# Kernel tuning notes

Hardware: AMD Instinct MI355X
Metric: run time of the kernel (lower is better)

The kernel has to match this reference:

```python
import jax, jax.numpy as jnp
import numpy as np

K_WIN = 7  # temporal window size (odd)
EPS = 1e-5


def setup_inputs() -> dict:
    key = jax.random.key(0)
    ks = jax.random.split(key, 10)
    B, C, T, H, W = 8, 512, 32, 7, 7
    N, E = 8, 64  # heads, inter channels = C // N
    s = 0.02
    return {
        "x": jax.random.normal(ks[0], (B, C, T, H, W), jnp.float32),
        "gamma": jnp.ones((C,), jnp.float32),
        "beta": jnp.zeros((C,), jnp.float32),
        "Wq": jax.random.normal(ks[1], (N, E, C), jnp.float32) * s,
        "bq": jax.random.normal(ks[2], (N, E), jnp.float32) * s,
        "Wk": jax.random.normal(ks[3], (N, E, C), jnp.float32) * s,
        "bk": jax.random.normal(ks[4], (N, E), jnp.float32) * s,
        "Wv": jax.random.normal(ks[5], (N, E, C), jnp.float32) * s,
        "bv": jax.random.normal(ks[6], (N, E), jnp.float32) * s,
        "Wo": jax.random.normal(ks[7], (N, C, E), jnp.float32) * s,
        "bo": jax.random.normal(ks[8], (N, C), jnp.float32) * s,
    }


def reference(x, gamma, beta, Wq, bq, Wk, bk, Wv, bv, Wo, bo):
    B, C, T, H, W = x.shape
    K = K_WIN
    P = H * W          # spatial positions per frame
    L = K * P          # positions per temporal window

    # BatchNorm3d (training-mode batch stats over B,T,H,W)
    mean = jnp.mean(x, axis=(0, 2, 3, 4), keepdims=True)
    var = jnp.var(x, axis=(0, 2, 3, 4), keepdims=True)
    g = gamma[None, :, None, None, None]
    b = beta[None, :, None, None, None]
    xb = g * (x - mean) * jax.lax.rsqrt(var + EPS) + b  # (B,C,T,H,W)

    # temporal zero-pad so that number of windows S == T
    pad = K // 2
    xp = jnp.pad(xb, ((0, 0), (0, 0), (pad, pad), (0, 0), (0, 0)))
    # gather sliding windows: (B,C,T,K,H,W)
    win_idx = jnp.arange(T)[:, None] + jnp.arange(K)[None, :]
    xw = xp[:, :, win_idx]

    xwf = xw.reshape(B, C, T, L)   # window tokens (key/value source)
    xcf = xb.reshape(B, C, T, P)   # center frame (query source)

    # per-head projections (dropout is identity in eval mode)
    q = jnp.einsum('nec,bctp->bntep', Wq, xcf) + bq[None, :, None, :, None]
    k = jnp.einsum('nec,bctl->bntel', Wk, xwf) + bk[None, :, None, :, None]
    v = jnp.einsum('nec,bctl->bntel', Wv, xwf) + bv[None, :, None, :, None]

    # attention: scores (B,N,T,P,L), softmax over window positions L (no scaling, as in original)
    alpha = jnp.einsum('bntep,bntel->bntpl', q, k)
    alpha = jax.nn.softmax(alpha, axis=-1)
    y = jnp.einsum('bntpl,bntel->bntep', alpha, v)

    # output projection per head, then mean over heads
    out = jnp.einsum('nce,bntep->bntcp', Wo, y) + bo[None, :, None, :, None]
    z = jnp.mean(out, axis=1)                 # (B,T,C,P)
    z = jnp.transpose(z, (0, 2, 1, 3)).reshape(B, C, T, H, W)
    return z + xb  # residual with BN output
```

## Files before the change

kernel.cpp:

```cpp
#include <hip/hip_runtime.h>
#include <hip/hip_bf16.h>


typedef float f32x4 __attribute__((ext_vector_type(4)));
typedef float f32x2 __attribute__((ext_vector_type(2)));
typedef short s16x8 __attribute__((ext_vector_type(8)));
typedef short s16x4 __attribute__((ext_vector_type(4)));
typedef __bf16 bf16x8 __attribute__((ext_vector_type(8)));

static __device__ __forceinline__ float bf2f(unsigned short u){
  union { unsigned int i; float f; } x; x.i = ((unsigned int)u) << 16; return x.f;
}
static __device__ __forceinline__ unsigned short f2bf(float f){
  union { __hip_bfloat16 h; unsigned short u; } x; x.h = __float2bfloat16(f); return x.u;
}
static __device__ __forceinline__ f32x4 mfma16(s16x8 a, s16x8 b, f32x4 c){
  return __builtin_amdgcn_mfma_f32_16x16x32_bf16(
      __builtin_bit_cast(bf16x8, a), __builtin_bit_cast(bf16x8, b), c, 0, 0, 0);
}
static __device__ __forceinline__ void gload16(const unsigned short* g, unsigned short* l){
  __builtin_amdgcn_global_load_lds(
      (const __attribute__((address_space(1))) unsigned int*)g,
      (__attribute__((address_space(3))) unsigned int*)l, 16, 0, 0);
}

__global__ __launch_bounds__(256) void xt_kernel(const float* __restrict__ x,
    unsigned short* __restrict__ Xt){
  __shared__ unsigned short Xc[512][53];
  const int bt = blockIdx.x, b = bt >> 5, t = bt & 31, tid = threadIdx.x;
  const float* xb = x + (size_t)b*802816 + t*49;
  for (int i = tid; i < 512*49; i += 256){
    int c = i / 49, p = i - c*49;
    Xc[c][p] = f2bf(xb[(size_t)c*1568 + p]);
  }
  __syncthreads();
  unsigned short* dst = Xt + (size_t)bt*49*512;
  for (int i = tid; i < 49*64; i += 256){
    int p = i >> 6, c0 = (i & 63) << 3;
    s16x8 v;
    #pragma unroll
    for (int j = 0; j < 8; ++j) v[j] = (short)Xc[c0+j][p];
    *(s16x8*)(dst + p*512 + c0) = v;
  }
}

__global__ __launch_bounds__(256) void stats1_kernel(const unsigned short* __restrict__ Xt,
    float* __restrict__ partials){
  __shared__ float R1[4][512];
  __shared__ float R2[4][512];
  const int blk = blockIdx.x, tid = threadIdx.x;
  const int rt = tid >> 6, c0 = (tid & 63)*8;
  const int r0 = blk*128;
  float s1[8] = {0,0,0,0,0,0,0,0}, s2[8] = {0,0,0,0,0,0,0,0};
  for (int r = rt; r < 128; r += 4){
    s16x8 v = *(const s16x8*)(Xt + (size_t)(r0 + r)*512 + c0);
    #pragma unroll
    for (int j = 0; j < 8; ++j){
      float f = bf2f((unsigned short)v[j]);
      s1[j] += f; s2[j] += f*f;
    }
  }
  #pragma unroll
  for (int j = 0; j < 8; ++j){ R1[rt][c0+j] = s1[j]; R2[rt][c0+j] = s2[j]; }
  __syncthreads();
  for (int c = tid; c < 512; c += 256){
    f32x2 o;
    o[0] = R1[0][c]+R1[1][c]+R1[2][c]+R1[3][c];
    o[1] = R2[0][c]+R2[1][c]+R2[2][c]+R2[3][c];
    *(f32x2*)(partials + ((size_t)blk*512 + c)*2) = o;
  }
}

__global__ __launch_bounds__(512) void stats2_kernel(const float* __restrict__ partials,
    const float* __restrict__ gamma, const float* __restrict__ beta,
    float* __restrict__ scale, float* __restrict__ shift){
  const int c = threadIdx.x;
  float s1 = 0.f, s2 = 0.f;
  for (int k = 0; k < 98; ++k){
    f32x2 v = *(const f32x2*)(partials + ((size_t)k*512 + c)*2);
    s1 += v[0]; s2 += v[1];
  }
  const float inv = 1.f/12544.f;
  float mean = s1*inv;
  float var  = s2*inv - mean*mean;
  float sc = gamma[c]*rsqrtf(var + 1e-5f);
  scale[c] = sc;
  shift[c] = beta[c] - mean*sc;
}

__global__ __launch_bounds__(512) void pack_kernel(const float* __restrict__ Wq,
    const float* __restrict__ Wk, const float* __restrict__ Wv,
    const float* __restrict__ Wo, const float* __restrict__ bo,
    const float* __restrict__ scale,
    unsigned short* __restrict__ Wall, unsigned short* __restrict__ Wo2,
    float* __restrict__ bo_sum){
  int i = blockIdx.x*512 + threadIdx.x;
  if (i < 786432){
    const float* W = (i < 262144) ? Wq : (i < 524288 ? Wk : Wv);
    Wall[i] = f2bf(W[i & 262143] * scale[i & 511]);
  } else if (i < 1048576){
    int j = i - 786432;
    int c = j >> 9, k = j & 511, nn = k >> 6, e = k & 63;
    Wo2[j] = f2bf(Wo[((size_t)nn*512 + c)*64 + e] * 0.125f);
  } else if (i < 1049088){
    int c = i - 1048576;
    float s = 0.f;
    #pragma unroll
    for (int nn = 0; nn < 8; ++nn) s += bo[nn*512 + c];
    bo_sum[c] = s * 0.125f;
  }
}

__global__ __launch_bounds__(64) void bias_kernel(const float* __restrict__ Wq,
    const float* __restrict__ Wk, const float* __restrict__ Wv,
    const float* __restrict__ bq, const float* __restrict__ bk,
    const float* __restrict__ bv, const float* __restrict__ shift,
    float* __restrict__ biasAll){
  const int row = blockIdx.x, lane = threadIdx.x;
  const float* W    = row < 512 ? Wq : (row < 1024 ? Wk : Wv);
  const float* bsrc = row < 512 ? bq : (row < 1024 ? bk : bv);
  const int r = row & 511;
  const float* Wr = W + (size_t)r*512;
  float s = 0.f;
  #pragma unroll
  for (int j = 0; j < 8; ++j) s += Wr[lane + 64*j]*shift[lane + 64*j];
  #pragma unroll
  for (int off = 32; off > 0; off >>= 1) s += __shfl_down(s, off);
  if (lane == 0) biasAll[row] = bsrc[r] + s;
}

__global__ __launch_bounds__(256) void qkv_gemm(const unsigned short* __restrict__ Wall,
    const unsigned short* __restrict__ Xt, const float* __restrict__ biasAll,
    unsigned short* __restrict__ Qg, unsigned short* __restrict__ Kg,
    unsigned short* __restrict__ Vg){
  __shared__ unsigned short As[2][4096];
  __shared__ unsigned short Bs[2][4096];
  const int bid = blockIdx.x;
  const int id = (bid & 7)*147 + (bid >> 3);
  const int bm = id % 12, bn = id / 12;
  const int m0 = bm*128, n0 = bn*128;
  const int tid = threadIdx.x;
  const int w = __builtin_amdgcn_readfirstlane(tid >> 6);
  const int lane = tid & 63, l15 = lane & 15, g = lane >> 4, g4 = (lane >> 4)*4;
  const int wm = w >> 1, wn = w & 1;
  const int cA = w*128 + lane;
  int offA[4], offB[4];
  #pragma unroll
  for (int mi = 0; mi < 4; ++mi){
    int row = wm*64 + mi*16 + l15;
    offA[mi] = row*32 + ((g ^ ((row>>1)&3))<<3);
  }
  #pragma unroll
  for (int ni = 0; ni < 4; ++ni){
    int col = wn*64 + ni*16 + l15;
    offB[ni] = col*32 + ((g ^ ((col>>1)&3))<<3);
  }
  f32x4 acc[4][4];
  #pragma unroll
  for (int mi = 0; mi < 4; ++mi)
    #pragma unroll
    for (int ni = 0; ni < 4; ++ni) acc[mi][ni] = 0.f;

  auto stage = [&](int bufi, int ks){
    #pragma unroll
    for (int it = 0; it < 2; ++it){
      int c = cA + it*64;
      int row = c >> 2, slot = c & 3;
      int ko = ks*32 + ((slot ^ ((row>>1)&3))<<3);
      gload16(Wall + (size_t)(m0 + row)*512 + ko, &As[bufi][(w*128 + it*64)*8]);
      gload16(Xt   + (size_t)(n0 + row)*512 + ko, &Bs[bufi][(w*128 + it*64)*8]);
    }
  };
  auto compute = [&](int bufi){
    s16x8 Af[4], Bf[4];
    #pragma unroll
    for (int mi = 0; mi < 4; ++mi) Af[mi] = *(const s16x8*)&As[bufi][offA[mi]];
    #pragma unroll
    for (int ni = 0; ni < 4; ++ni) Bf[ni] = *(const s16x8*)&Bs[bufi][offB[ni]];
    #pragma unroll
    for (int mi = 0; mi < 4; ++mi)
      #pragma unroll
      for (int ni = 0; ni < 4; ++ni)
        acc[mi][ni] = mfma16(Af[mi], Bf[ni], acc[mi][ni]);
  };

  stage(0, 0);
  __syncthreads();
  #pragma unroll 1
  for (int kk = 0; kk < 8; ++kk){
    stage(1, kk*2 + 1);
    compute(0);
    __syncthreads();
    if (kk < 7) stage(0, kk*2 + 2);
    compute(1);
    __syncthreads();
  }

  const int qb = bm*2 + wm;
  const int which = qb >> 3, n = qb & 7;
  f32x4 bb[4];
  #pragma unroll
  for (int mi = 0; mi < 4; ++mi)
    bb[mi] = *(const f32x4*)(biasAll + qb*64 + mi*16 + g4);
  #pragma unroll
  for (int ni = 0; ni < 4; ++ni){
    const int col = n0 + wn*64 + ni*16 + l15;
    const int btc = col / 49, p = col - btc*49;
    const size_t bnt = ((size_t)((btc >> 5)*8 + n)*32 + (btc & 31));
    #pragma unroll
    for (int mi = 0; mi < 4; ++mi){
      const int e0 = mi*16 + g4;
      f32x4 v = acc[mi][ni] + bb[mi];
      if (which == 0) v *= 1.4426950408889634f;
      if (which < 2){
        s16x4 u;
        #pragma unroll
        for (int r = 0; r < 4; ++r) u[r] = (short)f2bf(v[r]);
        *(s16x4*)((which == 0 ? Qg : Kg) + (bnt*49 + p)*64 + e0) = u;
      } else {
        #pragma unroll
        for (int r = 0; r < 4; ++r)
          Vg[bnt*3328 + (size_t)(e0 + r)*52 + p] = f2bf(v[r]);
      }
    }
  }
}

__global__ __launch_bounds__(512,2) void attn_kernel(const unsigned short* __restrict__ Qg,
    const unsigned short* __restrict__ Kg, const unsigned short* __restrict__ Vg,
    const float* __restrict__ bk, const float* __restrict__ bv,
    unsigned short* __restrict__ Yg){
  const int bid = blockIdx.x;
  const int bt = ((bid & 7) << 5) | (bid >> 3);
  const int b = bt >> 5, t = bt & 31, tid = threadIdx.x;
  const int n = __builtin_amdgcn_readfirstlane(tid >> 6);
  const int lane = tid & 63, g = lane >> 4, l15 = lane & 15, g4 = (lane >> 4)*4;
  const size_t bnt = ((size_t)(b*8 + n)*32 + t);
  const unsigned short* Qb = Qg + bnt*3136;
  s16x8 Qf[4][2];
  #pragma unroll
  for (int ni = 0; ni < 4; ++ni)
    #pragma unroll
    for (int ks = 0; ks < 2; ++ks)
      Qf[ni][ks] = *(const s16x8*)(Qb + (ni*16 + l15)*64 + ks*32 + g*8);
  const float* bkp = bk + n*64;
  f32x4 bkf[2][2];
  bkf[0][0] = *(const f32x4*)(bkp + g*8);      bkf[0][1] = *(const f32x4*)(bkp + g*8 + 4);
  bkf[1][0] = *(const f32x4*)(bkp + 32 + g*8); bkf[1][1] = *(const f32x4*)(bkp + 32 + g*8 + 4);
  float pad_l[4];
  #pragma unroll
  for (int ni = 0; ni < 4; ++ni){
    float s = 0.f;
    #pragma unroll
    for (int ks = 0; ks < 2; ++ks)
      #pragma unroll
      for (int h = 0; h < 2; ++h)
        #pragma unroll
        for (int j = 0; j < 4; ++j)
          s += bf2f((unsigned short)Qf[ni][ks][h*4+j]) * bkf[ks][h][j];
    s += __shfl_xor(s, 16); s += __shfl_xor(s, 32);
    pad_l[ni] = s;
  }
  float m_run[4], d_run[4];
  f32x4 Yacc[4][4];
  #pragma unroll
  for (int ni = 0; ni < 4; ++ni){
    m_run[ni] = -1e30f; d_run[ni] = 0.f;
    #pragma unroll
    for (int me = 0; me < 4; ++me) Yacc[me][ni] = 0.f;
  }
  int slo = 3 - t; if (slo < 0) slo = 0;
  int shi = 34 - t; if (shi > 6) shi = 6;
  for (int s = slo; s <= shi; ++s){
    const int tt = t + s - 3;
    const unsigned short* Kb = Kg + ((size_t)(b*8 + n)*32 + tt)*3136;
    const unsigned short* Vb = Vg + ((size_t)(b*8 + n)*32 + tt)*3328;
    f32x4 S[4][4];
    #pragma unroll
    for (int mi = 0; mi < 4; ++mi)
      #pragma unroll
      for (int ni = 0; ni < 4; ++ni) S[mi][ni] = 0.f;
    __builtin_amdgcn_s_setprio(1);
    #pragma unroll
    for (int ks = 0; ks < 2; ++ks)
      #pragma unroll
      for (int mi = 0; mi < 4; ++mi){
        s16x8 Kf = *(const s16x8*)(Kb + (mi*16 + l15)*64 + ks*32 + g*8);
        #pragma unroll
        for (int ni = 0; ni < 4; ++ni)
          S[mi][ni] = mfma16(Kf, Qf[ni][ks], S[mi][ni]);
      }
    __builtin_amdgcn_s_setprio(0);
    #pragma unroll
    for (int r = 0; r < 4; ++r){
      const bool bad = (g4 + r) >= 1;
      #pragma unroll
      for (int ni = 0; ni < 4; ++ni)
        S[3][ni][r] = bad ? -1e30f : S[3][ni][r];
    }
    #pragma unroll
    for (int ni = 0; ni < 4; ++ni){
      float mx = -1e30f;
      #pragma unroll
      for (int mi = 0; mi < 4; ++mi)
        #pragma unroll
        for (int r = 0; r < 4; ++r) mx = fmaxf(mx, S[mi][ni][r]);
      mx = fmaxf(mx, __shfl_xor(mx, 16));
      mx = fmaxf(mx, __shfl_xor(mx, 32));
      const float mn = fmaxf(m_run[ni], mx);
      const float rs = exp2f(m_run[ni] - mn);
      m_run[ni] = mn;
      float sum = 0.f;
      #pragma unroll
      for (int mi = 0; mi < 4; ++mi)
        #pragma unroll
        for (int r = 0; r < 4; ++r){
          float e = exp2f(S[mi][ni][r] - mn);
          S[mi][ni][r] = e; sum += e;
        }
      sum += __shfl_xor(sum, 16); sum += __shfl_xor(sum, 32);
      d_run[ni] = d_run[ni]*rs + sum;
      #pragma unroll
      for (int me = 0; me < 4; ++me) Yacc[me][ni] *= rs;
    }
    #pragma unroll
    for (int ks = 0; ks < 2; ++ks){
      s16x8 Pf[4];
      #pragma unroll
      for (int ni = 0; ni < 4; ++ni){
        f32x4 a = S[2*ks][ni], b2 = S[2*ks+1][ni];
        s16x8 pf;
        #pragma unroll
        for (int j = 0; j < 4; ++j){
          pf[j]   = (short)f2bf(a[j]);
          pf[4+j] = (short)f2bf(b2[j]);
        }
        Pf[ni] = pf;
      }
      __builtin_amdgcn_s_setprio(1);
      #pragma unroll
      for (int me = 0; me < 4; ++me){
        s16x4 vlo = *(const s16x4*)(Vb + (size_t)(me*16 + l15)*52 + ks*32 + g4);
        s16x4 vhi = *(const s16x4*)(Vb + (size_t)(me*16 + l15)*52 + ks*32 + 16 + g4);
        s16x8 Vf;
        #pragma unroll
        for (int j = 0; j < 4; ++j){ Vf[j] = vlo[j]; Vf[4+j] = vhi[j]; }
        #pragma unroll
        for (int ni = 0; ni < 4; ++ni)
          Yacc[me][ni] = mfma16(Vf, Pf[ni], Yacc[me][ni]);
      }
      __builtin_amdgcn_s_setprio(0);
    }
  }
  const int n_pad = slo + (6 - shi);
  f32x4 bvf[4];
  #pragma unroll
  for (int me = 0; me < 4; ++me)
    bvf[me] = *(const f32x4*)(bv + n*64 + me*16 + g4);
  unsigned short* Yb = Yg + bnt*3136;
  #pragma unroll
  for (int ni = 0; ni < 4; ++ni){
    float rs = 1.f, pw = 0.f, d = d_run[ni];
    if (n_pad > 0){
      const float mf = fmaxf(m_run[ni], pad_l[ni]);
      rs = exp2f(m_run[ni] - mf);
      pw = (float)(n_pad*49) * exp2f(pad_l[ni] - mf);
      d = d_run[ni]*rs + pw;
    }
    const float inv = 1.f/d;
    const int p = ni*16 + l15;
    if (p < 49){
      #pragma unroll
      for (int me = 0; me < 4; ++me){
        s16x4 u;
        #pragma unroll
        for (int r = 0; r < 4; ++r)
          u[r] = (short)f2bf((Yacc[me][ni][r]*rs + pw*bvf[me][r])*inv);
        *(s16x4*)(Yb + (size_t)p*64 + me*16 + g4) = u;
      }
    }
  }
}

__global__ __launch_bounds__(256) void out_gemm(const unsigned short* __restrict__ Wo2,
    const unsigned short* __restrict__ Yg, const unsigned short* __restrict__ Xt,
    const float* __restrict__ scale, const float* __restrict__ shift,
    const float* __restrict__ bo_sum, float* __restrict__ out){
  __shared__ unsigned short As[2][4096];
  __shared__ unsigned short Bs[2][4096];
  const int bid = blockIdx.x;
  const int id = (bid & 7)*49 + (bid >> 3);
  const int bm = id % 4, bn = id / 4;
  const int m0 = bm*128, n0 = bn*128;
  const int tid = threadIdx.x;
  const int w = __builtin_amdgcn_readfirstlane(tid >> 6);
  const int lane = tid & 63, l15 = lane & 15, g = lane >> 4, g4 = (lane >> 4)*4;
  const int wm = w >> 1, wn = w & 1;
  const int cA = w*128 + lane;
  int offA[4], offB[4];
  #pragma unroll
  for (int mi = 0; mi < 4; ++mi){
    int row = wm*64 + mi*16 + l15;
    offA[mi] = row*32 + ((g ^ ((row>>1)&3))<<3);
  }
  #pragma unroll
  for (int ni = 0; ni < 4; ++ni){
    int col = wn*64 + ni*16 + l15;
    offB[ni] = col*32 + ((g ^ ((col>>1)&3))<<3);
  }
  f32x4 acc[4][4];
  #pragma unroll
  for (int mi = 0; mi < 4; ++mi)
    #pragma unroll
    for (int ni = 0; ni < 4; ++ni) acc[mi][ni] = 0.f;

  auto stage = [&](int bufi, int ks){
    const int nh = ks >> 1, eo = (ks & 1)*32;
    #pragma unroll
    for (int it = 0; it < 2; ++it){
      int c = cA + it*64;
      int row = c >> 2, slot = c & 3;
      int sw = ((slot ^ ((row>>1)&3))<<3);
      gload16(Wo2 + (size_t)(m0 + row)*512 + ks*32 + sw, &As[bufi][(w*128 + it*64)*8]);
      const int col = n0 + row;
      const int btc = col / 49, p = col - btc*49;
      const size_t bb = ((size_t)((btc >> 5)*8 + nh)*32 + (btc & 31));
      gload16(Yg + bb*3136 + p*64 + eo + sw, &Bs[bufi][(w*128 + it*64)*8]);
    }
  };
  auto compute = [&](int bufi){
    s16x8 Af[4], Bf[4];
    #pragma unroll
    for (int mi = 0; mi < 4; ++mi) Af[mi] = *(const s16x8*)&As[bufi][offA[mi]];
    #pragma unroll
    for (int ni = 0; ni < 4; ++ni) Bf[ni] = *(const s16x8*)&Bs[bufi][offB[ni]];
    #pragma unroll
    for (int mi = 0; mi < 4; ++mi)
      #pragma unroll
      for (int ni = 0; ni < 4; ++ni)
        acc[mi][ni] = mfma16(Af[mi], Bf[ni], acc[mi][ni]);
  };

  stage(0, 0);
  __syncthreads();
  #pragma unroll 1
  for (int kk = 0; kk < 8; ++kk){
    stage(1, kk*2 + 1);
    compute(0);
    __syncthreads();
    if (kk < 7) stage(0, kk*2 + 2);
    compute(1);
    __syncthreads();
  }

  const int cb = m0 + wm*64;
  int colv[4]; size_t obase[4];
  #pragma unroll
  for (int ni = 0; ni < 4; ++ni){
    const int col = n0 + wn*64 + ni*16 + l15;
    const int btc = col / 49, p = col - btc*49;
    const int b = btc >> 5, t = btc & 31;
    colv[ni] = col;
    obase[ni] = (size_t)b*802816 + t*49 + p;
  }
  #pragma unroll
  for (int mi = 0; mi < 4; ++mi){
    const int c0 = cb + mi*16 + g4;
    const f32x4 bs = *(const f32x4*)(bo_sum + c0);
    const f32x4 sc = *(const f32x4*)(scale + c0);
    const f32x4 sh = *(const f32x4*)(shift + c0);
    #pragma unroll
    for (int ni = 0; ni < 4; ++ni){
      s16x4 xb = *(const s16x4*)(Xt + (size_t)colv[ni]*512 + c0);
      #pragma unroll
      for (int r = 0; r < 4; ++r){
        out[obase[ni] + (size_t)(c0 + r)*1568] =
            acc[mi][ni][r] + bs[r] + sc[r]*bf2f((unsigned short)xb[r]) + sh[r];
      }
    }
  }
}

extern "C" void kernel_launch(void* const* d_in, const int* in_sizes, int n_in_,
                              void* d_out, int out_size, void* d_ws, size_t ws_size,
                              hipStream_t stream){
  const float* x     = (const float*)d_in[0];
  const float* gamma = (const float*)d_in[1];
  const float* beta  = (const float*)d_in[2];
  const float* Wq    = (const float*)d_in[3];
  const float* bq    = (const float*)d_in[4];
  const float* Wk    = (const float*)d_in[5];
  const float* bk    = (const float*)d_in[6];
  const float* Wv    = (const float*)d_in[7];
  const float* bv    = (const float*)d_in[8];
  const float* Wo    = (const float*)d_in[9];
  const float* bo    = (const float*)d_in[10];
  float* out = (float*)d_out;

  char* ws = (char*)d_ws;
  float* scale    = (float*)ws;
  float* shift    = scale + 512;
  float* bo_sum   = shift + 512;
  float* biasAll  = bo_sum + 512;
  float* partials = biasAll + 1536;
  unsigned short* Wall = (unsigned short*)(ws + 417792);
  const size_t PAD = 16384;
  unsigned short* Wo2 = Wall + 786432;
  unsigned short* Xt  = Wo2 + 262144;
  unsigned short* Qg  = Xt + 6422528;
  unsigned short* Kg  = Qg + 6422528 + PAD;
  unsigned short* Vg  = Kg + 6422528 + PAD;
  unsigned short* Yg  = Vg + 6815744 + PAD;

  hipLaunchKernelGGL(xt_kernel, dim3(256), dim3(256), 0, stream, x, Xt);
  hipLaunchKernelGGL(stats1_kernel, dim3(98), dim3(256), 0, stream, Xt, partials);
  hipLaunchKernelGGL(stats2_kernel, dim3(1), dim3(512), 0, stream,
                     partials, gamma, beta, scale, shift);
  hipLaunchKernelGGL(pack_kernel, dim3(2049), dim3(512), 0, stream,
                     Wq, Wk, Wv, Wo, bo, scale, Wall, Wo2, bo_sum);
  hipLaunchKernelGGL(bias_kernel, dim3(1536), dim3(64), 0, stream,
                     Wq, Wk, Wv, bq, bk, bv, shift, biasAll);
  hipLaunchKernelGGL(qkv_gemm, dim3(1176), dim3(256), 0, stream,
                     Wall, Xt, biasAll, Qg, Kg, Vg);
  hipLaunchKernelGGL(attn_kernel, dim3(256), dim3(512), 0, stream,
                     Qg, Kg, Vg, bk, bv, Yg);
  hipLaunchKernelGGL(out_gemm, dim3(392), dim3(256), 0, stream,
                     Wo2, Yg, Xt, scale, shift, bo_sum, out);
}
```

Measured before the change: 137.1 us.

## Fuse stats and prep kernels, drop LDS staging in GEMMs, relayout Y

Folds the BatchNorm partial-sum pass into the transpose kernel and parallelises the final stats reduction across 8 blocks. Merges the weight-pack and bias kernels into one launch, cutting launch count. Both GEMMs lose their LDS double-buffered global_load_lds staging and load MFMA fragments straight from global memory. out_gemm moves to 64-thread single-wave blocks, and the attention output Y is written token-major so it can be read contiguously. This removes LDS traffic and barriers but relies on cache hits for reuse and may raise global load pressure.

Result: slower. 195.0 us (+42.3%).

```diff
diff --git a/kernel.cpp b/kernel.cpp
--- a/kernel.cpp
+++ b/kernel.cpp
@@ -18,14 +18,9 @@
   return __builtin_amdgcn_mfma_f32_16x16x32_bf16(
       __builtin_bit_cast(bf16x8, a), __builtin_bit_cast(bf16x8, b), c, 0, 0, 0);
 }
-static __device__ __forceinline__ void gload16(const unsigned short* g, unsigned short* l){
-  __builtin_amdgcn_global_load_lds(
-      (const __attribute__((address_space(1))) unsigned int*)g,
-      (__attribute__((address_space(3))) unsigned int*)l, 16, 0, 0);
-}
 
 __global__ __launch_bounds__(256) void xt_kernel(const float* __restrict__ x,
-    unsigned short* __restrict__ Xt){
+    unsigned short* __restrict__ Xt, float* __restrict__ partials){
   __shared__ unsigned short Xc[512][53];
   const int bt = blockIdx.x, b = bt >> 5, t = bt & 31, tid = threadIdx.x;
   const float* xb = x + (size_t)b*802816 + t*49;
@@ -42,99 +37,90 @@
     for (int j = 0; j < 8; ++j) v[j] = (short)Xc[c0+j][p];
     *(s16x8*)(dst + p*512 + c0) = v;
   }
-}
-
-__global__ __launch_bounds__(256) void stats1_kernel(const unsigned short* __restrict__ Xt,
-    float* __restrict__ partials){
-  __shared__ float R1[4][512];
-  __shared__ float R2[4][512];
-  const int blk = blockIdx.x, tid = threadIdx.x;
-  const int rt = tid >> 6, c0 = (tid & 63)*8;
-  const int r0 = blk*128;
-  float s1[8] = {0,0,0,0,0,0,0,0}, s2[8] = {0,0,0,0,0,0,0,0};
-  for (int r = rt; r < 128; r += 4){
-    s16x8 v = *(const s16x8*)(Xt + (size_t)(r0 + r)*512 + c0);
-    #pragma unroll
-    for (int j = 0; j < 8; ++j){
-      float f = bf2f((unsigned short)v[j]);
-      s1[j] += f; s2[j] += f*f;
-    }
-  }
-  #pragma unroll
-  for (int j = 0; j < 8; ++j){ R1[rt][c0+j] = s1[j]; R2[rt][c0+j] = s2[j]; }
-  __syncthreads();
   for (int c = tid; c < 512; c += 256){
-    f32x2 o;
-    o[0] = R1[0][c]+R1[1][c]+R1[2][c]+R1[3][c];
-    o[1] = R2[0][c]+R2[1][c]+R2[2][c]+R2[3][c];
-    *(f32x2*)(partials + ((size_t)blk*512 + c)*2) = o;
-  }
-}
-
-__global__ __launch_bounds__(512) void stats2_kernel(const float* __restrict__ partials,
+    float s1 = 0.f, s2 = 0.f;
+    #pragma unroll 7
+    for (int p = 0; p < 49; ++p){
+      float f = bf2f(Xc[c][p]);
+      s1 += f; s2 += f*f;
+    }
+    f32x2 o; o[0] = s1; o[1] = s2;
+    *(f32x2*)(partials + ((size_t)bt*512 + c)*2) = o;
+  }
+}
+
+__global__ __launch_bounds__(256) void stats2_kernel(const float* __restrict__ partials,
     const float* __restrict__ gamma, const float* __restrict__ beta,
     float* __restrict__ scale, float* __restrict__ shift){
-  const int c = threadIdx.x;
+  __shared__ float R1[4][64], R2[4][64];
+  const int h = blockIdx.x, tid = threadIdx.x;
+  const int r = tid >> 6, co = tid & 63;
+  const int c = h*64 + co;
   float s1 = 0.f, s2 = 0.f;
-  for (int k = 0; k < 98; ++k){
+  for (int k = r; k < 256; k += 4){
     f32x2 v = *(const f32x2*)(partials + ((size_t)k*512 + c)*2);
     s1 += v[0]; s2 += v[1];
   }
-  const float inv = 1.f/12544.f;
-  float mean = s1*inv;
-  float var  = s2*inv - mean*mean;
-  float sc = gamma[c]*rsqrtf(var + 1e-5f);
-  scale[c] = sc;
-  shift[c] = beta[c] - mean*sc;
-}
-
-__global__ __launch_bounds__(512) void pack_kernel(const float* __restrict__ Wq,
+  R1[r][co] = s1; R2[r][co] = s2;
+  __syncthreads();
+  if (tid < 64){
+    float t1 = R1[0][tid]+R1[1][tid]+R1[2][tid]+R1[3][tid];
+    float t2 = R2[0][tid]+R2[1][tid]+R2[2][tid]+R2[3][tid];
+    const int cc = h*64 + tid;
+    const float inv = 1.f/12544.f;
+    float mean = t1*inv;
+    float var  = t2*inv - mean*mean;
+    float sc = gamma[cc]*rsqrtf(var + 1e-5f);
+    scale[cc] = sc;
+    shift[cc] = beta[cc] - mean*sc;
+  }
+}
+
+__global__ __launch_bounds__(512) void prep_kernel(const float* __restrict__ Wq,
     const float* __restrict__ Wk, const float* __restrict__ Wv,
     const float* __restrict__ Wo, const float* __restrict__ bo,
-    const float* __restrict__ scale,
+    const float* __restrict__ bq, const float* __restrict__ bk,
+    const float* __restrict__ bv,
+    const float* __restrict__ scale, const float* __restrict__ shift,
     unsigned short* __restrict__ Wall, unsigned short* __restrict__ Wo2,
-    float* __restrict__ bo_sum){
-  int i = blockIdx.x*512 + threadIdx.x;
-  if (i < 786432){
-    const float* W = (i < 262144) ? Wq : (i < 524288 ? Wk : Wv);
-    Wall[i] = f2bf(W[i & 262143] * scale[i & 511]);
-  } else if (i < 1048576){
-    int j = i - 786432;
-    int c = j >> 9, k = j & 511, nn = k >> 6, e = k & 63;
-    Wo2[j] = f2bf(Wo[((size_t)nn*512 + c)*64 + e] * 0.125f);
-  } else if (i < 1049088){
-    int c = i - 1048576;
+    float* __restrict__ bo_sum, float* __restrict__ biasAll){
+  const int bid = blockIdx.x;
+  if (bid < 2049){
+    int i = bid*512 + threadIdx.x;
+    if (i < 786432){
+      const float* W = (i < 262144) ? Wq : (i < 524288 ? Wk : Wv);
+      Wall[i] = f2bf(W[i & 262143] * scale[i & 511]);
+    } else if (i < 1048576){
+      int j = i - 786432;
+      int c = j >> 9, k = j & 511, nn = k >> 6, e = k & 63;
+      Wo2[j] = f2bf(Wo[((size_t)nn*512 + c)*64 + e] * 0.125f);
+    } else if (i < 1049088){
+      int c = i - 1048576;
+      float s = 0.f;
+      #pragma unroll
+      for (int nn = 0; nn < 8; ++nn) s += bo[nn*512 + c];
+      bo_sum[c] = s * 0.125f;
+    }
+  } else {
+    const int row = (bid - 2049)*8 + (threadIdx.x >> 6);
+    const int lane = threadIdx.x & 63;
+    const float* W    = row < 512 ? Wq : (row < 1024 ? Wk : Wv);
+    const float* bsrc = row < 512 ? bq : (row < 1024 ? bk : bv);
+    const int r = row & 511;
+    const float* Wr = W + (size_t)r*512;
     float s = 0.f;
     #pragma unroll
-    for (int nn = 0; nn < 8; ++nn) s += bo[nn*512 + c];
-    bo_sum[c] = s * 0.125f;
-  }
-}
-
-__global__ __launch_bounds__(64) void bias_kernel(const float* __restrict__ Wq,
-    const float* __restrict__ Wk, const float* __restrict__ Wv,
-    const float* __restrict__ bq, const float* __restrict__ bk,
-    const float* __restrict__ bv, const float* __restrict__ shift,
-    float* __restrict__ biasAll){
-  const int row = blockIdx.x, lane = threadIdx.x;
-  const float* W    = row < 512 ? Wq : (row < 1024 ? Wk : Wv);
-  const float* bsrc = row < 512 ? bq : (row < 1024 ? bk : bv);
-  const int r = row & 511;
-  const float* Wr = W + (size_t)r*512;
-  float s = 0.f;
-  #pragma unroll
-  for (int j = 0; j < 8; ++j) s += Wr[lane + 64*j]*shift[lane + 64*j];
-  #pragma unroll
-  for (int off = 32; off > 0; off >>= 1) s += __shfl_down(s, off);
-  if (lane == 0) biasAll[row] = bsrc[r] + s;
-}
-
-__global__ __launch_bounds__(256) void qkv_gemm(const unsigned short* __restrict__ Wall,
+    for (int j = 0; j < 8; ++j) s += Wr[lane + 64*j]*shift[lane + 64*j];
+    #pragma unroll
+    for (int off = 32; off > 0; off >>= 1) s += __shfl_down(s, off);
+    if (lane == 0) biasAll[row] = bsrc[r] + s;
+  }
+}
+
+__global__ __launch_bounds__(256,2) void qkv_gemm(const unsigned short* __restrict__ Wall,
     const unsigned short* __restrict__ Xt, const float* __restrict__ biasAll,
     unsigned short* __restrict__ Qg, unsigned short* __restrict__ Kg,
     unsigned short* __restrict__ Vg){
-  __shared__ unsigned short As[2][4096];
-  __shared__ unsigned short Bs[2][4096];
   const int bid = blockIdx.x;
   const int id = (bid & 7)*147 + (bid >> 3);
   const int bm = id % 12, bn = id / 12;
@@ -143,59 +129,26 @@
   const int w = __builtin_amdgcn_readfirstlane(tid >> 6);
   const int lane = tid & 63, l15 = lane & 15, g = lane >> 4, g4 = (lane >> 4)*4;
   const int wm = w >> 1, wn = w & 1;
-  const int cA = w*128 + lane;
-  int offA[4], offB[4];
-  #pragma unroll
-  for (int mi = 0; mi < 4; ++mi){
-    int row = wm*64 + mi*16 + l15;
-    offA[mi] = row*32 + ((g ^ ((row>>1)&3))<<3);
-  }
-  #pragma unroll
-  for (int ni = 0; ni < 4; ++ni){
-    int col = wn*64 + ni*16 + l15;
-    offB[ni] = col*32 + ((g ^ ((col>>1)&3))<<3);
-  }
+  const unsigned short* Ab = Wall + (size_t)(m0 + wm*64 + l15)*512 + g*8;
+  const unsigned short* Bb = Xt   + (size_t)(n0 + wn*64 + l15)*512 + g*8;
   f32x4 acc[4][4];
   #pragma unroll
   for (int mi = 0; mi < 4; ++mi)
     #pragma unroll
     for (int ni = 0; ni < 4; ++ni) acc[mi][ni] = 0.f;
-
-  auto stage = [&](int bufi, int ks){
-    #pragma unroll
-    for (int it = 0; it < 2; ++it){
-      int c = cA + it*64;
-      int row = c >> 2, slot = c & 3;
-      int ko = ks*32 + ((slot ^ ((row>>1)&3))<<3);
-      gload16(Wall + (size_t)(m0 + row)*512 + ko, &As[bufi][(w*128 + it*64)*8]);
-      gload16(Xt   + (size_t)(n0 + row)*512 + ko, &Bs[bufi][(w*128 + it*64)*8]);
-    }
-  };
-  auto compute = [&](int bufi){
+  #pragma unroll 4
+  for (int ks = 0; ks < 16; ++ks){
     s16x8 Af[4], Bf[4];
     #pragma unroll
-    for (int mi = 0; mi < 4; ++mi) Af[mi] = *(const s16x8*)&As[bufi][offA[mi]];
-    #pragma unroll
-    for (int ni = 0; ni < 4; ++ni) Bf[ni] = *(const s16x8*)&Bs[bufi][offB[ni]];
+    for (int mi = 0; mi < 4; ++mi) Af[mi] = *(const s16x8*)(Ab + mi*8192 + ks*32);
+    #pragma unroll
+    for (int ni = 0; ni < 4; ++ni) Bf[ni] = *(const s16x8*)(Bb + ni*8192 + ks*32);
     #pragma unroll
     for (int mi = 0; mi < 4; ++mi)
       #pragma unroll
       for (int ni = 0; ni < 4; ++ni)
         acc[mi][ni] = mfma16(Af[mi], Bf[ni], acc[mi][ni]);
-  };
-
-  stage(0, 0);
-  __syncthreads();
-  #pragma unroll 1
-  for (int kk = 0; kk < 8; ++kk){
-    stage(1, kk*2 + 1);
-    compute(0);
-    __syncthreads();
-    if (kk < 7) stage(0, kk*2 + 2);
-    compute(1);
-    __syncthreads();
-  }
-
+  }
   const int qb = bm*2 + wm;
   const int which = qb >> 3, n = qb & 7;
   f32x4 bb[4];
@@ -357,7 +310,7 @@
   #pragma unroll
   for (int me = 0; me < 4; ++me)
     bvf[me] = *(const f32x4*)(bv + n*64 + me*16 + g4);
-  unsigned short* Yb = Yg + bnt*3136;
+  unsigned short* Yb = Yg + (size_t)bt*49*512 + n*64;
   #pragma unroll
   for (int ni = 0; ni < 4; ++ni){
     float rs = 1.f, pw = 0.f, d = d_run[ni];
@@ -376,88 +329,45 @@
         #pragma unroll
         for (int r = 0; r < 4; ++r)
           u[r] = (short)f2bf((Yacc[me][ni][r]*rs + pw*bvf[me][r])*inv);
-        *(s16x4*)(Yb + (size_t)p*64 + me*16 + g4) = u;
-      }
-    }
-  }
-}
-
-__global__ __launch_bounds__(256) void out_gemm(const unsigned short* __restrict__ Wo2,
+        *(s16x4*)(Yb + (size_t)p*512 + me*16 + g4) = u;
+      }
+    }
+  }
+}
+
+__global__ __launch_bounds__(64,2) void out_gemm(const unsigned short* __restrict__ Wo2,
     const unsigned short* __restrict__ Yg, const unsigned short* __restrict__ Xt,
     const float* __restrict__ scale, const float* __restrict__ shift,
     const float* __restrict__ bo_sum, float* __restrict__ out){
-  __shared__ unsigned short As[2][4096];
-  __shared__ unsigned short Bs[2][4096];
   const int bid = blockIdx.x;
-  const int id = (bid & 7)*49 + (bid >> 3);
-  const int bm = id % 4, bn = id / 4;
-  const int m0 = bm*128, n0 = bn*128;
-  const int tid = threadIdx.x;
-  const int w = __builtin_amdgcn_readfirstlane(tid >> 6);
-  const int lane = tid & 63, l15 = lane & 15, g = lane >> 4, g4 = (lane >> 4)*4;
-  const int wm = w >> 1, wn = w & 1;
-  const int cA = w*128 + lane;
-  int offA[4], offB[4];
-  #pragma unroll
-  for (int mi = 0; mi < 4; ++mi){
-    int row = wm*64 + mi*16 + l15;
-    offA[mi] = row*32 + ((g ^ ((row>>1)&3))<<3);
-  }
-  #pragma unroll
-  for (int ni = 0; ni < 4; ++ni){
-    int col = wn*64 + ni*16 + l15;
-    offB[ni] = col*32 + ((g ^ ((col>>1)&3))<<3);
-  }
+  const int id = (bid & 7)*196 + (bid >> 3);
+  const int mt = id % 8, nt = id / 8;
+  const int m0 = mt*64, n0 = nt*64;
+  const int lane = threadIdx.x & 63, l15 = lane & 15, g = lane >> 4, g4 = (lane >> 4)*4;
+  const unsigned short* Ab = Wo2 + (size_t)(m0 + l15)*512 + g*8;
+  const unsigned short* Bb = Yg  + (size_t)(n0 + l15)*512 + g*8;
   f32x4 acc[4][4];
   #pragma unroll
   for (int mi = 0; mi < 4; ++mi)
     #pragma unroll
     for (int ni = 0; ni < 4; ++ni) acc[mi][ni] = 0.f;
-
-  auto stage = [&](int bufi, int ks){
-    const int nh = ks >> 1, eo = (ks & 1)*32;
-    #pragma unroll
-    for (int it = 0; it < 2; ++it){
-      int c = cA + it*64;
-      int row = c >> 2, slot = c & 3;
-      int sw = ((slot ^ ((row>>1)&3))<<3);
-      gload16(Wo2 + (size_t)(m0 + row)*512 + ks*32 + sw, &As[bufi][(w*128 + it*64)*8]);
-      const int col = n0 + row;
-      const int btc = col / 49, p = col - btc*49;
-      const size_t bb = ((size_t)((btc >> 5)*8 + nh)*32 + (btc & 31));
-      gload16(Yg + bb*3136 + p*64 + eo + sw, &Bs[bufi][(w*128 + it*64)*8]);
-    }
-  };
-  auto compute = [&](int bufi){
+  #pragma unroll 4
+  for (int ks = 0; ks < 16; ++ks){
     s16x8 Af[4], Bf[4];
     #pragma unroll
-    for (int mi = 0; mi < 4; ++mi) Af[mi] = *(const s16x8*)&As[bufi][offA[mi]];
-    #pragma unroll
-    for (int ni = 0; ni < 4; ++ni) Bf[ni] = *(const s16x8*)&Bs[bufi][offB[ni]];
+    for (int mi = 0; mi < 4; ++mi) Af[mi] = *(const s16x8*)(Ab + mi*8192 + ks*32);
+    #pragma unroll
+    for (int ni = 0; ni < 4; ++ni) Bf[ni] = *(const s16x8*)(Bb + ni*8192 + ks*32);
     #pragma unroll
     for (int mi = 0; mi < 4; ++mi)
       #pragma unroll
       for (int ni = 0; ni < 4; ++ni)
         acc[mi][ni] = mfma16(Af[mi], Bf[ni], acc[mi][ni]);
-  };
-
-  stage(0, 0);
-  __syncthreads();
-  #pragma unroll 1
-  for (int kk = 0; kk < 8; ++kk){
-    stage(1, kk*2 + 1);
-    compute(0);
-    __syncthreads();
-    if (kk < 7) stage(0, kk*2 + 2);
-    compute(1);
-    __syncthreads();
-  }
-
-  const int cb = m0 + wm*64;
+  }
   int colv[4]; size_t obase[4];
   #pragma unroll
   for (int ni = 0; ni < 4; ++ni){
-    const int col = n0 + wn*64 + ni*16 + l15;
+    const int col = n0 + ni*16 + l15;
     const int btc = col / 49, p = col - btc*49;
     const int b = btc >> 5, t = btc & 31;
     colv[ni] = col;
@@ -465,7 +375,7 @@
   }
   #pragma unroll
   for (int mi = 0; mi < 4; ++mi){
-    const int c0 = cb + mi*16 + g4;
+    const int c0 = m0 + mi*16 + g4;
     const f32x4 bs = *(const f32x4*)(bo_sum + c0);
     const f32x4 sc = *(const f32x4*)(scale + c0);
     const f32x4 sh = *(const f32x4*)(shift + c0);
@@ -503,7 +413,7 @@
   float* bo_sum   = shift + 512;
   float* biasAll  = bo_sum + 512;
   float* partials = biasAll + 1536;
-  unsigned short* Wall = (unsigned short*)(ws + 417792);
+  unsigned short* Wall = (unsigned short*)(ws + 1064960);
   const size_t PAD = 16384;
   unsigned short* Wo2 = Wall + 786432;
   unsigned short* Xt  = Wo2 + 262144;
@@ -512,18 +422,16 @@
   unsigned short* Vg  = Kg + 6422528 + PAD;
   unsigned short* Yg  = Vg + 6815744 + PAD;
 
-  hipLaunchKernelGGL(xt_kernel, dim3(256), dim3(256), 0, stream, x, Xt);
-  hipLaunchKernelGGL(stats1_kernel, dim3(98), dim3(256), 0, stream, Xt, partials);
-  hipLaunchKernelGGL(stats2_kernel, dim3(1), dim3(512), 0, stream,
+  hipLaunchKernelGGL(xt_kernel, dim3(256), dim3(256), 0, stream, x, Xt, partials);
+  hipLaunchKernelGGL(stats2_kernel, dim3(8), dim3(256), 0, stream,
                      partials, gamma, beta, scale, shift);
-  hipLaunchKernelGGL(pack_kernel, dim3(2049), dim3(512), 0, stream,
-                     Wq, Wk, Wv, Wo, bo, scale, Wall, Wo2, bo_sum);
-  hipLaunchKernelGGL(bias_kernel, dim3(1536), dim3(64), 0, stream,
-                     Wq, Wk, Wv, bq, bk, bv, shift, biasAll);
+  hipLaunchKernelGGL(prep_kernel, dim3(2241), dim3(512), 0, stream,
+                     Wq, Wk, Wv, Wo, bo, bq, bk, bv, scale, shift,
+                     Wall, Wo2, bo_sum, biasAll);
   hipLaunchKernelGGL(qkv_gemm, dim3(1176), dim3(256), 0, stream,
                      Wall, Xt, biasAll, Qg, Kg, Vg);
   hipLaunchKernelGGL(attn_kernel, dim3(256), dim3(512), 0, stream,
                      Qg, Kg, Vg, bk, bv, Yg);
-  hipLaunchKernelGGL(out_gemm, dim3(392), dim3(256), 0, stream,
+  hipLaunchKernelGGL(out_gemm, dim3(1568), dim3(64), 0, stream,
                      Wo2, Yg, Xt, scale, shift, bo_sum, out);
 }
```
